# Optimization experiments

Measured on AMD Instinct MI355X. Metric: run time of the kernel, lower is better.

The kernel has to match this reference:

```python
import jax, jax.numpy as jnp
import numpy as np

B, L, C, H = 8, 2048, 256, 4
D = C // H  # head_dim = 64
EPS = 1e-5


def setup_inputs() -> dict:
    key = jax.random.key(0)
    ks = jax.random.split(key, 16)
    s = lambda fan_in: 1.0 / np.sqrt(fan_in)
    inp = {
        'x0': jax.random.normal(ks[0], (B, L, C), jnp.float32),
        'x1': jax.random.normal(ks[1], (B, L, C), jnp.float32),
        # attention projections (stored as (in, out); torch Linear is x @ W.T + b)
        'Wqk': jax.random.normal(ks[2], (C, C), jnp.float32) * s(C),
        'bqk': jax.random.normal(ks[3], (C,), jnp.float32) * s(C),
        'Wv': jax.random.normal(ks[4], (C, C), jnp.float32) * s(C),
        'bv': jax.random.normal(ks[5], (C,), jnp.float32) * s(C),
        'Wout': jax.random.normal(ks[6], (C, C), jnp.float32) * s(C),
        'bout': jax.random.normal(ks[7], (C,), jnp.float32) * s(C),
        # shared FFN: Linear(2C->2C) -> LayerNorm -> GELU -> Linear(2C->C)
        'W1': jax.random.normal(ks[8], (2 * C, 2 * C), jnp.float32) * s(2 * C),
        'b1': jax.random.normal(ks[9], (2 * C,), jnp.float32) * s(2 * C),
        'ln_g': jnp.ones((2 * C,), jnp.float32),
        'ln_b': jnp.zeros((2 * C,), jnp.float32),
        'W2': jax.random.normal(ks[10], (2 * C, C), jnp.float32) * s(2 * C),
        'b2': jax.random.normal(ks[11], (C,), jnp.float32) * s(2 * C),
    }
    return inp


def _heads(t):
    # (B, L, C) -> (B, H, L, D)
    b, l, _ = t.shape
    return t.reshape(b, l, H, D).transpose(0, 2, 1, 3)


def _merge(t):
    # (B, H, L, D) -> (B, L, C)
    b, h, l, d = t.shape
    return t.transpose(0, 2, 1, 3).reshape(b, l, h * d)


def _ffn(z, W1, b1, ln_g, ln_b, W2, b2):
    h = z @ W1 + b1
    mu = jnp.mean(h, axis=-1, keepdims=True)
    var = jnp.var(h, axis=-1, keepdims=True)
    h = (h - mu) * jax.lax.rsqrt(var + EPS) * ln_g + ln_b
    h = jax.nn.gelu(h, approximate=False)
    return h @ W2 + b2


def reference(x0, x1, Wqk, bqk, Wv, bv, Wout, bout, W1, b1, ln_g, ln_b, W2, b2):
    scale_sqrt = D ** (-0.25)  # sqrt(head_dim**-0.5), applied to both sides
    qk0 = _heads(x0 @ Wqk + bqk) * scale_sqrt  # (B,H,M,D)
    qk1 = _heads(x1 @ Wqk + bqk) * scale_sqrt  # (B,H,N,D)
    v0 = _heads(x0 @ Wv + bv)
    v1 = _heads(x1 @ Wv + bv)

    # single shared similarity matrix (LightGlue trick)
    sim = jnp.einsum('bhid,bhjd->bhij', qk0, qk1)  # (B,H,M,N)
    attn01 = jax.nn.softmax(sim, axis=-1)           # rows: A->B
    attn10 = jax.nn.softmax(sim, axis=-2)           # cols: B->A (softmax of sim^T along last dim)
    m0 = jnp.einsum('bhij,bhjd->bhid', attn01, v1)  # (B,H,M,D)
    m1 = jnp.einsum('bhij,bhid->bhjd', attn10, v0)  # (B,H,N,D)

    m0 = _merge(m0) @ Wout + bout
    m1 = _merge(m1) @ Wout + bout

    x0_out = x0 + _ffn(jnp.concatenate([x0, m0], axis=-1), W1, b1, ln_g, ln_b, W2, b2)
    x1_out = x1 + _ffn(jnp.concatenate([x1, m1], axis=-1), W1, b1, ln_g, ln_b, W2, b2)
    return (x0_out, x1_out)
```

## Files before the change

kernel.cpp:

```cpp
#include <hip/hip_runtime.h>
#include <hip/hip_bf16.h>

typedef _Float16 f16;
typedef _Float16 f16x8 __attribute__((ext_vector_type(8)));
typedef _Float16 f16x4 __attribute__((ext_vector_type(4)));
typedef float f32x4 __attribute__((ext_vector_type(4)));

#define MFMA16(a, b, c) __builtin_amdgcn_mfma_f32_16x16x32_f16((a), (b), (c), 0, 0, 0)
#define MFMA16K16(a, b, c) __builtin_amdgcn_mfma_f32_16x16x16f16((a), (b), (c), 0, 0, 0)

__device__ __forceinline__ void load16(const void* g, void* l) {
    __builtin_amdgcn_global_load_lds((const __attribute__((address_space(1))) void*)g,
                                     (__attribute__((address_space(3))) void*)l, 16, 0, 0);
}

__global__ __launch_bounds__(256) void k_prep(const float* __restrict__ x0,
                                              const float* __restrict__ x1,
                                              const float* __restrict__ Wqk,
                                              const float* __restrict__ Wv,
                                              const float* __restrict__ W1,
                                              const float* __restrict__ W2,
                                              const float* __restrict__ Wout,
                                              const float* __restrict__ b1,
                                              const float* __restrict__ bout,
                                              f16* __restrict__ xh, f16* __restrict__ wcat_t,
                                              f16* __restrict__ w1t, f16* __restrict__ w1bt,
                                              f16* __restrict__ w2t, f16* __restrict__ woutf16,
                                              float* __restrict__ bias_eff) {
    __shared__ float red[4];
    const int blk = blockIdx.x, tid = threadIdx.x;
    if (blk < 8192) {
        size_t i = ((size_t)blk * 256 + tid) * 4;
        const float* src = (i < 4194304) ? (x0 + i) : (x1 + (i - 4194304));
        float4 v = *(const float4*)src;
        f16x4 o = {(f16)v.x, (f16)v.y, (f16)v.z, (f16)v.w};
        *(f16x4*)(xh + i) = o;
    } else if (blk < 8704) {
        int n = blk - 8192;
        const float* W = (n < 256) ? Wqk : Wv;
        wcat_t[n * 256 + tid] = (f16)W[tid * 256 + (n & 255)];
    } else if (blk < 9216) {
        int n = blk - 8704;
        w1t[n * 512 + tid] = (f16)W1[tid * 512 + n];
    } else if (blk < 9728) {
        int n = blk - 9216;
        w1bt[n * 256 + tid] = (f16)W1[(256 + tid) * 512 + n];
    } else if (blk < 10240) {
        int j = blk - 9728;
        int n = j >> 1, k = (j & 1) * 256 + tid;
        w2t[n * 512 + k] = (f16)W2[k * 256 + n];
    } else if (blk < 10496) {
        int o = (blk - 10240) * 256 + tid;
        woutf16[o] = (f16)Wout[o];
    } else {
        int n = blk - 10496;
        float s = bout[tid] * W1[(size_t)(256 + tid) * 512 + n];
#pragma unroll
        for (int off = 1; off < 64; off <<= 1) s += __shfl_xor(s, off);
        int wave = tid >> 6, lane = tid & 63;
        if (lane == 0) red[wave] = s;
        __syncthreads();
        if (tid == 0) bias_eff[n] = b1[n] + red[0] + red[1] + red[2] + red[3];
    }
}

__global__ __launch_bounds__(256, 2) void k_gemm(const f16* __restrict__ A1,
                                                 const f16* __restrict__ A2, int ksplit,
                                                 int strideA, const f16* __restrict__ Bt, int K,
                                                 int N, const float* __restrict__ bias1,
                                                 const float* __restrict__ bias2, int mode,
                                                 void* __restrict__ out1, void* __restrict__ out2,
                                                 const f16* __restrict__ resh) {
    const int bm0 = blockIdx.x * 128;
    const int bn0 = blockIdx.y * 256;
    __shared__ f16 As[2][4096];
    __shared__ f16 Bs[2][8192];
    const int tid = threadIdx.x;
    const int lane = tid & 63, wave = tid >> 6;
    const int quad = lane >> 4, l16 = lane & 15;
    const int wm0 = (wave & 1) * 64, wn0 = (wave >> 1) * 128;
    const int axor = l16 & 3;

    f32x4 acc[4][8];
#pragma unroll
    for (int tm = 0; tm < 4; tm++)
#pragma unroll
        for (int tn = 0; tn < 8; tn++) acc[tm][tn] = (f32x4){0.f, 0.f, 0.f, 0.f};

    auto stage = [&](int buf, int kt) {
        const int k0 = kt * 32;
        const f16* Ab = (k0 < ksplit) ? A1 : A2;
        const int koff = (k0 < ksplit) ? k0 : k0 - ksplit;
#pragma unroll
        for (int rd = 0; rd < 2; rd++) {
            const int cbase = rd * 256 + wave * 64;
            const int c = cbase + lane;
            const int row = c >> 2, col = (c & 3) ^ (row & 3);
            load16(Ab + (size_t)(bm0 + row) * strideA + koff + col * 8, &As[buf][cbase * 8]);
        }
#pragma unroll
        for (int rd = 0; rd < 4; rd++) {
            const int cbase = rd * 256 + wave * 64;
            const int c = cbase + lane;
            const int row = c >> 2, col = (c & 3) ^ (row & 3);
            load16(Bt + (size_t)(bn0 + row) * K + k0 + col * 8, &Bs[buf][cbase * 8]);
        }
    };

    const int NT = K >> 5;
    stage(0, 0);
    __syncthreads();
    for (int kt = 0; kt < NT; kt++) {
        const int cur = kt & 1;
        if (kt + 1 < NT) stage(cur ^ 1, kt + 1);
        f16x8 af[4], bf[8];
#pragma unroll
        for (int t = 0; t < 4; t++)
            af[t] = *(const f16x8*)&As[cur][(wm0 + t * 16 + l16) * 32 + (quad ^ axor) * 8];
#pragma unroll
        for (int t = 0; t < 8; t++)
            bf[t] = *(const f16x8*)&Bs[cur][(wn0 + t * 16 + l16) * 32 + (quad ^ axor) * 8];
#pragma unroll
        for (int tm = 0; tm < 4; tm++)
#pragma unroll
            for (int tn = 0; tn < 8; tn++) acc[tm][tn] = MFMA16(bf[tn], af[tm], acc[tm][tn]);
        __syncthreads();
    }

#pragma unroll
    for (int tm = 0; tm < 4; tm++) {
        const int m = bm0 + wm0 + tm * 16 + l16;
#pragma unroll
        for (int tn = 0; tn < 8; tn++) {
            const int n = bn0 + wn0 + tn * 16 + quad * 4;
            f32x4 v = acc[tm][tn];
            if (mode == 0) {
                const int s = m >> 14, r14 = m & 16383, b = r14 >> 11, l = r14 & 2047;
                if (n < 256) {
                    float4 bi = *(const float4*)(bias1 + n);
                    const int h = n >> 6, d = n & 63;
                    const size_t hh = (size_t)((s * 8 + b) * 4 + h);
                    f16x4 o = {(f16)((v[0] + bi.x) * 0.42466090f),
                               (f16)((v[1] + bi.y) * 0.42466090f),
                               (f16)((v[2] + bi.z) * 0.42466090f),
                               (f16)((v[3] + bi.w) * 0.42466090f)};
                    *(f16x4*)((f16*)out1 + (hh * 2048 + l) * 64 + d) = o;
                } else {
                    const int n2 = n - 256;
                    float4 bi = *(const float4*)(bias2 + n2);
                    const int h = n2 >> 6, d = n2 & 63;
                    const size_t hh = (size_t)((s * 8 + b) * 4 + h);
                    f16* o2 = (f16*)out2 + (hh * 64 + d) * 2048 + l;
                    o2[0] = (f16)(v[0] + bi.x);
                    o2[2048] = (f16)(v[1] + bi.y);
                    o2[4096] = (f16)(v[2] + bi.z);
                    o2[6144] = (f16)(v[3] + bi.w);
                }
            } else if (mode == 2) {
                float4 bi = *(const float4*)(bias1 + n);
                f16x4 o = {(f16)(v[0] + bi.x), (f16)(v[1] + bi.y), (f16)(v[2] + bi.z),
                           (f16)(v[3] + bi.w)};
                *(f16x4*)((f16*)out1 + (size_t)m * N + n) = o;
            } else if (mode == 3) {
                float4 bi = *(const float4*)(bias1 + n);
                f16x4 rr = *(const f16x4*)(resh + (size_t)m * 256 + n);
                float4 o = {v[0] + bi.x + (float)rr[0], v[1] + bi.y + (float)rr[1],
                            v[2] + bi.z + (float)rr[2], v[3] + bi.w + (float)rr[3]};
                *(float4*)((float*)out1 + (size_t)m * 256 + n) = o;
            } else {
                f16x4 o = {(f16)v[0], (f16)v[1], (f16)v[2], (f16)v[3]};
                *(f16x4*)((f16*)out1 + (size_t)m * 512 + 256 + n) = o;
            }
        }
    }
}

__global__ __launch_bounds__(256, 4) void k_flash(const f16* __restrict__ qkbuf,
                                                  const f16* __restrict__ vtbuf,
                                                  f16* __restrict__ mbuf) {
    const int z = blockIdx.z;
    const int bh = blockIdx.x;
    const int qt = blockIdx.y;
    const size_t HSZ = 2048 * 64;
    const size_t SSZ = 32 * HSZ;
    const f16* Q = qkbuf + (z ? SSZ : 0) + bh * HSZ;
    const f16* Kp = qkbuf + (z ? 0 : SSZ) + bh * HSZ;
    const f16* Vt = vtbuf + (z ? 0 : SSZ) + bh * HSZ;
    f16* Mo = mbuf + (size_t)z * (16384 * 256);

    __shared__ f16 Ks[2][4096];
    __shared__ f16 Vs[2][4096];

    const int tid = threadIdx.x, lane = tid & 63, wave = tid >> 6;
    const int quad = lane >> 4, l16 = lane & 15;
    const int srow = lane >> 3;
    const int slc = (lane & 7) ^ (srow & 7);

    const int q0 = qt * 128 + wave * 32;
    f16x8 qf[2][2];
#pragma unroll
    for (int tq = 0; tq < 2; tq++)
#pragma unroll
        for (int kk = 0; kk < 2; kk++)
            qf[tq][kk] =
                *(const f16x8*)(Q + (size_t)(q0 + tq * 16 + l16) * 64 + kk * 32 + quad * 8);

    auto stage = [&](int buf, int kv0) {
#pragma unroll
        for (int i = 0; i < 2; i++) {
            const int widx = wave * 2 + i;
            const int row = widx * 8 + srow;
            load16(Kp + (size_t)(kv0 + row) * 64 + slc * 8, &Ks[buf][widx * 512]);
            load16(Vt + (size_t)row * 2048 + kv0 + slc * 8, &Vs[buf][widx * 512]);
        }
    };

    f32x4 oacc[4][2];
#pragma unroll
    for (int td = 0; td < 4; td++)
#pragma unroll
        for (int tq = 0; tq < 2; tq++) oacc[td][tq] = (f32x4){0.f, 0.f, 0.f, 0.f};
    float lrow[2] = {0.f, 0.f};

    stage(0, 0);
    __syncthreads();

    for (int t = 0; t < 32; t++) {
        const int cur = t & 1;
        if (t < 31) stage(cur ^ 1, (t + 1) * 64);
        const f16* Kc = Ks[cur];
        const f16* Vc = Vs[cur];

        f32x4 sacc[4][2];
#pragma unroll
        for (int tkv = 0; tkv < 4; tkv++)
#pragma unroll
            for (int tq = 0; tq < 2; tq++) sacc[tkv][tq] = (f32x4){0.f, 0.f, 0.f, 0.f};
#pragma unroll
        for (int kk = 0; kk < 2; kk++) {
#pragma unroll
            for (int tkv = 0; tkv < 4; tkv++) {
                const int r = tkv * 16 + l16;
                f16x8 ka = *(const f16x8*)(Kc + r * 64 + (((kk * 4 + quad) ^ (r & 7)) * 8));
#pragma unroll
                for (int tq = 0; tq < 2; tq++)
                    sacc[tkv][tq] = MFMA16(ka, qf[tq][kk], sacc[tkv][tq]);
            }
        }

        f16x4 pk[4][2];
#pragma unroll
        for (int tq = 0; tq < 2; tq++) {
            float rs = 0.f;
#pragma unroll
            for (int tkv = 0; tkv < 4; tkv++) {
                float p0 = __builtin_amdgcn_exp2f(sacc[tkv][tq][0] - 8.0f);
                float p1 = __builtin_amdgcn_exp2f(sacc[tkv][tq][1] - 8.0f);
                float p2 = __builtin_amdgcn_exp2f(sacc[tkv][tq][2] - 8.0f);
                float p3 = __builtin_amdgcn_exp2f(sacc[tkv][tq][3] - 8.0f);
                pk[tkv][tq] = (f16x4){(f16)p0, (f16)p1, (f16)p2, (f16)p3};
                rs += (p0 + p1) + (p2 + p3);
            }
            lrow[tq] += rs;
        }

#pragma unroll
        for (int tkv = 0; tkv < 4; tkv++) {
#pragma unroll
            for (int td = 0; td < 4; td++) {
                const int r = td * 16 + l16;
                f16x4 va = *(const f16x4*)(Vc + r * 64 +
                                           (((2 * tkv + (quad >> 1)) ^ (r & 7)) * 8) +
                                           (quad & 1) * 4);
#pragma unroll
                for (int tq = 0; tq < 2; tq++)
                    oacc[td][tq] = MFMA16K16(va, pk[tkv][tq], oacc[td][tq]);
            }
        }
        __syncthreads();
    }

    const int b = bh >> 2, h = bh & 3;
#pragma unroll
    for (int tq = 0; tq < 2; tq++) {
        float ls = lrow[tq];
        ls += __shfl_xor(ls, 16);
        ls += __shfl_xor(ls, 32);
        const float inv = 1.f / ls;
        const int q = q0 + tq * 16 + l16;
        const size_t base = ((size_t)(b * 2048 + q)) * 256 + h * 64;
#pragma unroll
        for (int td = 0; td < 4; td++) {
            f16x4 o = {(f16)(oacc[td][tq][0] * inv), (f16)(oacc[td][tq][1] * inv),
                       (f16)(oacc[td][tq][2] * inv), (f16)(oacc[td][tq][3] * inv)};
            *(f16x4*)(Mo + base + td * 16 + quad * 4) = o;
        }
    }
}

__global__ __launch_bounds__(256) void k_ln_gelu(f16* __restrict__ h,
                                                 const float* __restrict__ g,
                                                 const float* __restrict__ bb) {
    const int tid = threadIdx.x, wave = tid >> 6, lane = tid & 63;
    const size_t row = (size_t)blockIdx.x * 4 + wave;
    f16* hr = h + row * 512 + lane * 8;
    f16x8 v = *(const f16x8*)hr;
    float x[8];
    float s = 0.f, sq = 0.f;
#pragma unroll
    for (int i = 0; i < 8; i++) {
        x[i] = (float)v[i];
        s += x[i];
        sq += x[i] * x[i];
    }
#pragma unroll
    for (int off = 1; off < 64; off <<= 1) {
        s += __shfl_xor(s, off);
        sq += __shfl_xor(sq, off);
    }
    const float mu = s * (1.f / 512.f);
    const float var = sq * (1.f / 512.f) - mu * mu;
    const float rstd = rsqrtf(var + 1e-5f);
    float4 g0 = *(const float4*)(g + lane * 8), g1 = *(const float4*)(g + lane * 8 + 4);
    float4 b0 = *(const float4*)(bb + lane * 8), b1 = *(const float4*)(bb + lane * 8 + 4);
    float gg[8] = {g0.x, g0.y, g0.z, g0.w, g1.x, g1.y, g1.z, g1.w};
    float bv[8] = {b0.x, b0.y, b0.z, b0.w, b1.x, b1.y, b1.z, b1.w};
#pragma unroll
    for (int i = 0; i < 8; i++) {
        float a = (x[i] - mu) * rstd * gg[i] + bv[i];
        a = 0.5f * a * (1.f + erff(a * 0.70710678118f));
        v[i] = (f16)a;
    }
    *(f16x8*)hr = v;
}


extern "C" void kernel_launch(void* const* d_in, const int* in_sizes, int n_in, void* d_out,
                              int out_size, void* d_ws, size_t ws_size, hipStream_t stream) {
    const float* x0 = (const float*)d_in[0];
    const float* x1 = (const float*)d_in[1];
    const float* Wqk = (const float*)d_in[2];
    const float* bqk = (const float*)d_in[3];
    const float* Wv = (const float*)d_in[4];
    const float* bv = (const float*)d_in[5];
    const float* Wout = (const float*)d_in[6];
    const float* bout = (const float*)d_in[7];
    const float* W1 = (const float*)d_in[8];
    const float* b1 = (const float*)d_in[9];
    const float* lng = (const float*)d_in[10];
    const float* lnb = (const float*)d_in[11];
    const float* W2 = (const float*)d_in[12];
    const float* b2 = (const float*)d_in[13];
    float* out = (float*)d_out;

    char* ws = (char*)d_ws;
    f16* xh = (f16*)(ws);
    f16* qk = (f16*)(ws + 16777216);
    f16* vt = (f16*)(ws + 33554432);
    f16* mbuf = (f16*)(ws + 50331648);
    f16* hbuf = qk;
    f16* w1bt = (f16*)(ws + 16777216);
    f16* woutf16 = w1bt + 131072;
    f16* wcat_t = (f16*)(ws + 67108864);
    f16* w1t = wcat_t + 131072;
    f16* w2t = w1t + 262144;
    float* bias_eff = (float*)(w2t + 131072);

    k_prep<<<11008, 256, 0, stream>>>(x0, x1, Wqk, Wv, W1, W2, Wout, b1, bout, xh, wcat_t, w1t,
                                      w1bt, w2t, woutf16, bias_eff);
    k_gemm<<<dim3(4, 1), 256, 0, stream>>>(w1bt, w1bt, 1 << 30, 256, woutf16, 256, 256, nullptr,
                                           nullptr, 4, w1t, nullptr, nullptr);
    k_gemm<<<dim3(256, 2), 256, 0, stream>>>(xh, xh, 1 << 30, 256, wcat_t, 256, 512, bqk, bv, 0,
                                             qk, vt, nullptr);
    k_flash<<<dim3(32, 16, 2), 256, 0, stream>>>(qk, vt, mbuf);
    k_gemm<<<dim3(256, 2), 256, 0, stream>>>(xh, mbuf, 256, 256, w1t, 512, 512, bias_eff,
                                             nullptr, 2, hbuf, nullptr, nullptr);
    k_ln_gelu<<<8192, 256, 0, stream>>>(hbuf, lng, lnb);
    k_gemm<<<dim3(256, 1), 256, 0, stream>>>(hbuf, hbuf, 1 << 30, 512, w2t, 512, 256, b2,
                                             nullptr, 3, out, nullptr, xh);
}
```

Baseline: 318.2 us.

## Tile weight transposes in prep and relax GEMM waitcnt to overlap loads

Weight transposes in the prep kernel now go through 64x64 LDS tiles, so both the reads and the writes are coalesced. Previously each block did strided single-column gathers, and the grid shrinks accordingly. The bias_eff reduction moves to a single block doing a serial dot product. In the GEMM main loop, the full __syncthreads (which drains all outstanding loads) is replaced with an explicit s_waitcnt vmcnt(6) plus a raw s_barrier, so the next stage's loads stay in flight during compute. The vmcnt constant assumes exactly 6 async loads per stage and relies on hand-written ordering for correctness.

```diff
diff --git a/kernel.cpp b/kernel.cpp
--- a/kernel.cpp
+++ b/kernel.cpp
@@ -27,40 +27,67 @@
                                               f16* __restrict__ w1t, f16* __restrict__ w1bt,
                                               f16* __restrict__ w2t, f16* __restrict__ woutf16,
                                               float* __restrict__ bias_eff) {
-    __shared__ float red[4];
     const int blk = blockIdx.x, tid = threadIdx.x;
-    if (blk < 8192) {
-        size_t i = ((size_t)blk * 256 + tid) * 4;
+    if (blk < 128) {
+        __shared__ float tile[64][65];
+        const float* src;
+        f16* dst;
+        int sStride, dStride, r0, c0;
+        if (blk < 16) {
+            int ti = blk >> 2, tj = blk & 3;
+            src = Wqk; sStride = 256; dst = wcat_t; dStride = 256;
+            r0 = ti * 64; c0 = tj * 64;
+        } else if (blk < 32) {
+            int j = blk - 16; int ti = j >> 2, tj = j & 3;
+            src = Wv; sStride = 256; dst = wcat_t + 65536; dStride = 256;
+            r0 = ti * 64; c0 = tj * 64;
+        } else if (blk < 64) {
+            int j = blk - 32; int ti = j >> 3, tj = j & 7;
+            src = W1; sStride = 512; dst = w1t; dStride = 512;
+            r0 = ti * 64; c0 = tj * 64;
+        } else if (blk < 96) {
+            int j = blk - 64; int ti = j >> 3, tj = j & 7;
+            src = W1 + 256 * 512; sStride = 512; dst = w1bt; dStride = 256;
+            r0 = ti * 64; c0 = tj * 64;
+        } else {
+            int j = blk - 96; int ti = j >> 2, tj = j & 3;
+            src = W2; sStride = 256; dst = w2t; dStride = 512;
+            r0 = ti * 64; c0 = tj * 64;
+        }
+        const int lane = tid & 63, grp = tid >> 6;
+#pragma unroll 4
+        for (int it = 0; it < 16; it++) {
+            int rr = grp + it * 4;
+            tile[rr][lane] = src[(size_t)(r0 + rr) * sStride + c0 + lane];
+        }
+        __syncthreads();
+#pragma unroll 4
+        for (int it = 0; it < 16; it++) {
+            int cc = grp + it * 4;
+            dst[(size_t)(c0 + cc) * dStride + r0 + lane] = (f16)tile[lane][cc];
+        }
+    } else if (blk < 192) {
+        int o = (blk - 128) * 1024 + tid * 4;
+        float4 v = *(const float4*)(Wout + o);
+        f16x4 q = {(f16)v.x, (f16)v.y, (f16)v.z, (f16)v.w};
+        *(f16x4*)(woutf16 + o) = q;
+    } else if (blk == 192) {
+        float a0 = b1[tid], a1 = b1[tid + 256];
+#pragma unroll 4
+        for (int j = 0; j < 256; j++) {
+            const float* row = W1 + (size_t)(256 + j) * 512;
+            float bj = bout[j];
+            a0 += bj * row[tid];
+            a1 += bj * row[tid + 256];
+        }
+        bias_eff[tid] = a0;
+        bias_eff[tid + 256] = a1;
+    } else {
+        size_t i = ((size_t)(blk - 193) * 256 + tid) * 4;
         const float* src = (i < 4194304) ? (x0 + i) : (x1 + (i - 4194304));
         float4 v = *(const float4*)src;
         f16x4 o = {(f16)v.x, (f16)v.y, (f16)v.z, (f16)v.w};
         *(f16x4*)(xh + i) = o;
-    } else if (blk < 8704) {
-        int n = blk - 8192;
-        const float* W = (n < 256) ? Wqk : Wv;
-        wcat_t[n * 256 + tid] = (f16)W[tid * 256 + (n & 255)];
-    } else if (blk < 9216) {
-        int n = blk - 8704;
-        w1t[n * 512 + tid] = (f16)W1[tid * 512 + n];
-    } else if (blk < 9728) {
-        int n = blk - 9216;
-        w1bt[n * 256 + tid] = (f16)W1[(256 + tid) * 512 + n];
-    } else if (blk < 10240) {
-        int j = blk - 9728;
-        int n = j >> 1, k = (j & 1) * 256 + tid;
-        w2t[n * 512 + k] = (f16)W2[k * 256 + n];
-    } else if (blk < 10496) {
-        int o = (blk - 10240) * 256 + tid;
-        woutf16[o] = (f16)Wout[o];
-    } else {
-        int n = blk - 10496;
-        float s = bout[tid] * W1[(size_t)(256 + tid) * 512 + n];
-#pragma unroll
-        for (int off = 1; off < 64; off <<= 1) s += __shfl_xor(s, off);
-        int wave = tid >> 6, lane = tid & 63;
-        if (lane == 0) red[wave] = s;
-        __syncthreads();
-        if (tid == 0) bias_eff[n] = b1[n] + red[0] + red[1] + red[2] + red[3];
     }
 }
 
@@ -109,10 +136,15 @@
 
     const int NT = K >> 5;
     stage(0, 0);
-    __syncthreads();
     for (int kt = 0; kt < NT; kt++) {
         const int cur = kt & 1;
-        if (kt + 1 < NT) stage(cur ^ 1, kt + 1);
+        if (kt + 1 < NT) {
+            stage(cur ^ 1, kt + 1);
+            asm volatile("s_waitcnt vmcnt(6)" ::: "memory");
+        } else {
+            asm volatile("s_waitcnt vmcnt(0)" ::: "memory");
+        }
+        asm volatile("s_barrier" ::: "memory");
         f16x8 af[4], bf[8];
 #pragma unroll
         for (int t = 0; t < 4; t++)
@@ -124,7 +156,7 @@
         for (int tm = 0; tm < 4; tm++)
 #pragma unroll
             for (int tn = 0; tn < 8; tn++) acc[tm][tn] = MFMA16(bf[tn], af[tm], acc[tm][tn]);
-        __syncthreads();
+        asm volatile("s_barrier" ::: "memory");
     }
 
 #pragma unroll
@@ -366,8 +398,8 @@
     f16* w2t = w1t + 262144;
     float* bias_eff = (float*)(w2t + 131072);
 
-    k_prep<<<11008, 256, 0, stream>>>(x0, x1, Wqk, Wv, W1, W2, Wout, b1, bout, xh, wcat_t, w1t,
-                                      w1bt, w2t, woutf16, bias_eff);
+    k_prep<<<8385, 256, 0, stream>>>(x0, x1, Wqk, Wv, W1, W2, Wout, b1, bout, xh, wcat_t, w1t,
+                                     w1bt, w2t, woutf16, bias_eff);
     k_gemm<<<dim3(4, 1), 256, 0, stream>>>(w1bt, w1bt, 1 << 30, 256, woutf16, 256, 256, nullptr,
                                            nullptr, 4, w1t, nullptr, nullptr);
     k_gemm<<<dim3(256, 2), 256, 0, stream>>>(xh, xh, 1 << 30, 256, wcat_t, 256, 512, bqk, bv, 0,
```

Result: slower. 328.2 us (+3.2%).
